# Optimization experiments

Measured on AMD Instinct MI355X. Metric: run time of the kernel, lower is better.

The kernel has to match this reference:

```python
import jax, jax.numpy as jnp
import numpy as np

TAU = 0.07          # temperature
TOP_N_SIM = 5       # n_neighb for KNN label assignment
RANKING_K = 4       # top-k same/diff-class sims for confidence ratio


def setup_inputs() -> dict:
    key = jax.random.key(0)
    k1, k2, k3 = jax.random.split(key, 3)
    n_src, n_tgt, d, n_cls = 8192, 6144, 256, 64
    return {
        "source_features": jax.random.normal(k1, (n_src, d), dtype=jnp.float32),
        "source_labels": jax.random.randint(k2, (n_src,), 0, n_cls, dtype=jnp.int32),
        "target_features": jax.random.normal(k3, (n_tgt, d), dtype=jnp.float32),
    }


def _l2_normalize(x):
    # F.normalize(x, dim=1, p=2) with eps=1e-12
    n = jnp.sqrt(jnp.sum(x * x, axis=1, keepdims=True))
    return x / jnp.maximum(n, 1e-12)


def reference(source_features, source_labels, target_features):
    n_tgt = target_features.shape[0]
    top_ranked_n = n_tgt * 2 // 3

    # cosine similarity matrix [n_src, n_tgt]
    sim = _l2_normalize(source_features) @ _l2_normalize(target_features).T

    # sort each column descending over sources
    order = jnp.argsort(-sim, axis=0)                      # [S, T]

    # KNN label assignment with torch.mode semantics (tie -> smallest value)
    neigh = source_labels[order[:TOP_N_SIM]]               # [K, T]
    counts = (neigh[:, None, :] == neigh[None, :, :]).sum(axis=1)  # [K, T]
    maxc = counts.max(axis=0)                              # [T]
    big = jnp.iinfo(source_labels.dtype).max
    assigned = jnp.where(counts == maxc[None, :], neigh, big).min(axis=0)  # [T]

    # sims & labels reordered by descending similarity, per column
    sorted_sims = jnp.take_along_axis(sim, order, axis=0)  # [S, T]
    sorted_labels = source_labels[order]                   # [S, T]
    pos = sorted_labels == assigned[None, :]               # [S, T]

    def first_k_masked_sum(mask):
        # sum of first RANKING_K sorted sims where mask is True, per column
        csum = jnp.cumsum(mask.astype(sim.dtype), axis=0)
        sel = mask & (csum <= RANKING_K)
        return jnp.sum(jnp.where(sel, sorted_sims, 0.0), axis=0)

    nln = first_k_masked_sum(pos)
    nun = first_k_masked_sum(~pos)
    scores = jax.lax.stop_gradient(nln / nun)              # [T], detached

    _, top_ind = jax.lax.top_k(scores, top_ranked_n)       # confident targets
    conf_sim = sim[:, top_ind]                             # [S, top_ranked_n]
    conf_lab = assigned[top_ind]

    # contrastive softmax loss over sources
    mask_sim = (source_labels[:, None] == conf_lab[None, :]).astype(sim.dtype)
    exp_scores = jax.nn.softmax(conf_sim / TAU, axis=0)
    contrastive = (exp_scores * mask_sim).sum(axis=0) / exp_scores.sum(axis=0)
    return -jnp.mean(jnp.log(contrastive + 1e-6))
```

## Files before the change

### kernel.cpp

```cpp
#include <hip/hip_runtime.h>
#include <cstdint>
#include <cstddef>

#define DIM 256
#define NSRC 8192
#define NCLS 64
#define KSTEPS 8
#define INV_TAU (1.0f / 0.07f)
#define EPITCH 136

typedef __attribute__((ext_vector_type(8))) short bf16x8;
typedef __attribute__((ext_vector_type(4))) float f32x4;
typedef unsigned char uchar;

__device__ __forceinline__ ushort f2bf_rne(float f) {
    uint u = __float_as_uint(f);
    uint r = u + 0x7fff + ((u >> 16) & 1);
    return (ushort)(r >> 16);
}
__device__ __forceinline__ uint bf2ord(uint u) {
    return u ^ (0x8000u + (u >> 15) * 0x7FFFu);
}
__device__ __forceinline__ float ord2f(uint o) {
    uint u = (o & 0x8000u) ? (o ^ 0x8000u) : (~o & 0xFFFFu);
    return __uint_as_float(u << 16);
}

__device__ __forceinline__ void gload_lds16(const void* g, void* l) {
    __builtin_amdgcn_global_load_lds((const __attribute__((address_space(1))) void*)g,
                                     (__attribute__((address_space(3))) void*)l,
                                     16, 0, 0);
}

__global__ __launch_bounds__(256) void l2bf2_k(const float* __restrict__ inA,
                                               ushort* __restrict__ outA, int nA,
                                               const float* __restrict__ inB,
                                               ushort* __restrict__ outB, int nB) {
    const int w = (blockIdx.x * 256 + threadIdx.x) >> 6;
    const int lane = threadIdx.x & 63;
    if (w >= nA + nB) return;
    const float* in;
    ushort* out;
    int row;
    if (w < nA) { in = inA; out = outA; row = w; }
    else        { in = inB; out = outB; row = w - nA; }
    float4 v = *(const float4*)(in + (size_t)row * DIM + lane * 4);
    float ss = v.x * v.x + v.y * v.y + v.z * v.z + v.w * v.w;
#pragma unroll
    for (int d = 1; d < 64; d <<= 1) ss += __shfl_xor(ss, d);
    const float n = fmaxf(sqrtf(ss), 1e-12f);
    ushort4 o;
    o.x = f2bf_rne(v.x / n);
    o.y = f2bf_rne(v.y / n);
    o.z = f2bf_rne(v.z / n);
    o.w = f2bf_rne(v.w / n);
    *(ushort4*)(out + (size_t)row * DIM + lane * 4) = o;
}

__global__ __launch_bounds__(256) void class_build_k(const int* __restrict__ labels,
                                                     uchar* __restrict__ lab8,
                                                     int* __restrict__ cstart,
                                                     int* __restrict__ clist, int n) {
    const int c = blockIdx.x, t = threadIdx.x;
    const int g = c * 256 + t;
    if (g < n) lab8[g] = (uchar)labels[g];

    __shared__ int sl[256], se[256];
    const int per = n >> 8;
    const int i0 = t * per;
    int less = 0, eq = 0;
    for (int j = 0; j < per; ++j) {
        const int l = labels[i0 + j];
        less += (l < c);
        eq += (l == c);
    }
    sl[t] = less; se[t] = eq;
    __syncthreads();
    for (int s = 1; s < 256; s <<= 1) {
        const int a = (t >= s) ? sl[t - s] : 0;
        const int b = (t >= s) ? se[t - s] : 0;
        __syncthreads();
        sl[t] += a; se[t] += b;
        __syncthreads();
    }
    const int base = sl[255];
    int pos = base + se[t] - eq;
    for (int j = 0; j < per; ++j) {
        const int i = i0 + j;
        if (labels[i] == c) clist[pos++] = i;
    }
    if (t == 0) cstart[c] = base;
    if (c == 0 && t == 1) cstart[NCLS] = n;
}

__global__ __launch_bounds__(256) void gemm_mfma_k(const ushort* __restrict__ A,
                                                   const ushort* __restrict__ B,
                                                   ushort* __restrict__ C,
                                                   int M, int N) {
    __shared__ __align__(16) ushort smem[32768];

    const int tid = threadIdx.x;
    const int lane = tid & 63, wid = tid >> 6;
    const int wr = wid >> 1, wc = wid & 1;

    const int nwg = gridDim.x * gridDim.y;
    const int bid = blockIdx.y * gridDim.x + blockIdx.x;
    const int cpx = nwg >> 3;
    const int swzb = (bid & 7) * cpx + (bid >> 3);
    const int bm = (swzb / gridDim.x) * 128;
    const int bn = (swzb % gridDim.x) * 128;

    const char* aSrc[2];
    const char* bSrc[2];
    uint ldsOff[2];
#pragma unroll
    for (int it = 0; it < 2; ++it) {
        const int c = it * 256 + tid;
        const int r = c >> 2;
        const int ch = c & 3;
        const int sch = ch ^ ((r >> 1) & 3);
        aSrc[it] = (const char*)A + (size_t)(bm + r) * (DIM * 2) + sch * 16;
        bSrc[it] = (const char*)B + (size_t)(bn + r) * (DIM * 2) + sch * 16;
        ldsOff[it] = it * 4096 + (uint)(wid * 1024);
    }

    const int fr = lane & 15, fk = lane >> 4;
    const int swz = (fr >> 1) & 3;
    int idxA[4], idxB[4];
#pragma unroll
    for (int m = 0; m < 4; ++m)
        idxA[m] = (wr * 64 + m * 16 + fr) * 32 + ((fk ^ swz) * 8);
#pragma unroll
    for (int n = 0; n < 4; ++n)
        idxB[n] = (wc * 64 + n * 16 + fr) * 32 + ((fk ^ swz) * 8);

    f32x4 acc[4][4];
#pragma unroll
    for (int m = 0; m < 4; ++m)
#pragma unroll
        for (int n = 0; n < 4; ++n) acc[m][n] = (f32x4){0.f, 0.f, 0.f, 0.f};

#define STAGE(b, ks)                                                               \
    {                                                                              \
        _Pragma("unroll") for (int it = 0; it < 2; ++it) {                         \
            gload_lds16(aSrc[it] + (ks) * 64,                                      \
                        (char*)smem + (b) * 8192 + ldsOff[it]);                    \
            gload_lds16(bSrc[it] + (ks) * 64,                                      \
                        (char*)smem + 32768 + (b) * 8192 + ldsOff[it]);            \
        }                                                                          \
    }

    STAGE(0, 0);
    STAGE(1, 1);
    STAGE(2, 2);

#pragma unroll
    for (int ks = 0; ks < KSTEPS; ++ks) {
        if (ks < KSTEPS - 2)      { asm volatile("s_waitcnt vmcnt(8)" ::: "memory"); }
        else if (ks == KSTEPS - 2){ asm volatile("s_waitcnt vmcnt(4)" ::: "memory"); }
        else                      { asm volatile("s_waitcnt vmcnt(0)" ::: "memory"); }
        __builtin_amdgcn_s_barrier();
        asm volatile("" ::: "memory");

        if (ks + 3 < KSTEPS) STAGE((ks + 3) & 3, ks + 3);

        const ushort* sAc = smem + (ks & 3) * 4096;
        const ushort* sBc = smem + 16384 + (ks & 3) * 4096;
        bf16x8 av[4], bv[4];
#pragma unroll
        for (int m = 0; m < 4; ++m) av[m] = *(const bf16x8*)&sAc[idxA[m]];
#pragma unroll
        for (int n = 0; n < 4; ++n) bv[n] = *(const bf16x8*)&sBc[idxB[n]];
#pragma unroll
        for (int m = 0; m < 4; ++m)
#pragma unroll
            for (int n = 0; n < 4; ++n)
                acc[m][n] = __builtin_amdgcn_mfma_f32_16x16x32_bf16(av[m], bv[n], acc[m][n], 0, 0, 0);
    }
#undef STAGE

    __syncthreads();
#pragma unroll
    for (int m = 0; m < 4; ++m) {
#pragma unroll
        for (int n = 0; n < 4; ++n) {
            const int colb = wc * 64 + n * 16 + fr;
#pragma unroll
            for (int j = 0; j < 4; ++j) {
                const int rowb = wr * 64 + m * 16 + fk * 4 + j;
                smem[rowb * EPITCH + colb] = (ushort)bf2ord((uint)f2bf_rne(acc[m][n][j]));
            }
        }
    }
    __syncthreads();
    const int rr = tid >> 4, cc = (tid & 15) * 8;
#pragma unroll
    for (int it = 0; it < 8; ++it) {
        const int r = it * 16 + rr;
        uint4 v = *(const uint4*)&smem[r * EPITCH + cc];
        *(uint4*)(C + (size_t)(bm + r) * N + bn + cc) = v;
    }
}

__global__ __launch_bounds__(256) void assign_score_w(const ushort* __restrict__ sim,
                                                      const int* __restrict__ labels,
                                                      const uchar* __restrict__ lab8,
                                                      const int* __restrict__ cstart,
                                                      const int* __restrict__ clist,
                                                      float* __restrict__ scores_out,
                                                      float* __restrict__ logt_out) {
    const int lane = threadIdx.x & 63, wid = threadIdx.x >> 6;
    const int t = blockIdx.x * 4 + wid;
    const ushort* row = sim + (size_t)t * NSRC;

    uint k0 = 0, k1 = 0, k2 = 0, k3 = 0, k4 = 0, k5 = 0, k6 = 0, k7 = 0;
    float s1 = 0.f;

#define CH4(u16, idx)                                                   \
    {                                                                   \
        uint uu = (uint)(u16);                                          \
        s1 += __expf(fmaf(ord2f(uu), INV_TAU, -INV_TAU));               \
        uint nk = (uu << 16) | (uint)(8191 - (idx));                    \
        uint q;                                                         \
        q = max(k0, nk); nk = min(k0, nk); k0 = q;                      \
        q = max(k1, nk); nk = min(k1, nk); k1 = q;                      \
        q = max(k2, nk); nk = min(k2, nk); k2 = q;                      \
        k3 = max(k3, nk);                                               \
    }
#define CH8(u16, idx)                                                   \
    {                                                                   \
        uint nk = (((uint)(u16)) << 16) | (uint)(8191 - (idx));         \
        uint q;                                                         \
        q = max(k0, nk); nk = min(k0, nk); k0 = q;                      \
        q = max(k1, nk); nk = min(k1, nk); k1 = q;                      \
        q = max(k2, nk); nk = min(k2, nk); k2 = q;                      \
        q = max(k3, nk); nk = min(k3, nk); k3 = q;                      \
        q = max(k4, nk); nk = min(k4, nk); k4 = q;                      \
        q = max(k5, nk); nk = min(k5, nk); k5 = q;                      \
        q = max(k6, nk); nk = min(k6, nk); k6 = q;                      \
        k7 = max(k7, nk);                                               \
    }
#define MERGE8                                                                     \
    _Pragma("unroll")                                                              \
    for (int d = 1; d < 64; d <<= 1) {                                             \
        uint b0 = __shfl_xor(k0, d), b1 = __shfl_xor(k1, d), b2 = __shfl_xor(k2, d),\
             b3 = __shfl_xor(k3, d), b4 = __shfl_xor(k4, d), b5 = __shfl_xor(k5, d),\
             b6 = __shfl_xor(k6, d), b7 = __shfl_xor(k7, d);                        \
        uint r0 = max(k0, b0);                                                     \
        uint r1 = max(max(min(k0, b0), k1), b1);                                   \
        uint r2 = max(max(min(k0, b1), min(k1, b0)), max(k2, b2));                 \
        uint r3 = max(max(min(k0, b2), min(k1, b1)),                               \
                      max(max(min(k2, b0), k3), b3));                              \
        uint r4 = max(max(max(min(k0, b3), min(k1, b2)),                           \
                          max(min(k2, b1), min(k3, b0))), max(k4, b4));            \
        uint r5 = max(max(max(min(k0, b4), min(k1, b3)),                           \
                          max(min(k2, b2), min(k3, b1))),                          \
                      max(max(min(k4, b0), k5), b5));                              \
        uint r6 = max(max(max(min(k0, b5), min(k1, b4)),                           \
                          max(min(k2, b3), min(k3, b2))),                          \
                      max(max(min(k4, b1), min(k5, b0)), max(k6, b6)));            \
        uint r7 = max(max(max(min(k0, b6), min(k1, b5)),                           \
                          max(min(k2, b4), min(k3, b3))),                          \
                      max(max(min(k4, b2), min(k5, b1)),                           \
                          max(max(min(k6, b0), k7), b7)));                         \
        k0 = r0; k1 = r1; k2 = r2; k3 = r3; k4 = r4; k5 = r5; k6 = r6; k7 = r7;    \
    }

    for (int i0 = lane * 8; i0 < NSRC; i0 += 512) {
        uint4 w = *(const uint4*)(row + i0);
        CH4(w.x & 0xFFFF, i0 + 0); CH4(w.x >> 16, i0 + 1);
        CH4(w.y & 0xFFFF, i0 + 2); CH4(w.y >> 16, i0 + 3);
        CH4(w.z & 0xFFFF, i0 + 4); CH4(w.z >> 16, i0 + 5);
        CH4(w.w & 0xFFFF, i0 + 6); CH4(w.w >> 16, i0 + 7);
    }
    const uint prek3 = k3;
    MERGE8;
    if (!__all((int)(prek3 <= k7))) {
        k0 = k1 = k2 = k3 = k4 = k5 = k6 = k7 = 0;
        for (int i0 = lane * 8; i0 < NSRC; i0 += 512) {
            uint4 w = *(const uint4*)(row + i0);
            CH8(w.x & 0xFFFF, i0 + 0); CH8(w.x >> 16, i0 + 1);
            CH8(w.y & 0xFFFF, i0 + 2); CH8(w.y >> 16, i0 + 3);
            CH8(w.z & 0xFFFF, i0 + 4); CH8(w.z >> 16, i0 + 5);
            CH8(w.w & 0xFFFF, i0 + 6); CH8(w.w >> 16, i0 + 7);
        }
        MERGE8;
    }
#undef CH4
#undef CH8
#undef MERGE8

#pragma unroll
    for (int d = 1; d < 64; d <<= 1) s1 += __shfl_xor(s1, d);

    const int l0 = labels[8191 - (int)(k0 & 0xFFFF)];
    const int l1 = labels[8191 - (int)(k1 & 0xFFFF)];
    const int l2 = labels[8191 - (int)(k2 & 0xFFFF)];
    const int l3 = labels[8191 - (int)(k3 & 0xFFFF)];
    const int l4 = labels[8191 - (int)(k4 & 0xFFFF)];
    const int l5 = labels[8191 - (int)(k5 & 0xFFFF)];
    const int l6 = labels[8191 - (int)(k6 & 0xFFFF)];
    const int l7 = labels[8191 - (int)(k7 & 0xFFFF)];

    const int c0 = 1 + (l0 == l1) + (l0 == l2) + (l0 == l3) + (l0 == l4);
    const int c1 = (l1 == l0) + 1 + (l1 == l2) + (l1 == l3) + (l1 == l4);
    const int c2 = (l2 == l0) + (l2 == l1) + 1 + (l2 == l3) + (l2 == l4);
    const int c3 = (l3 == l0) + (l3 == l1) + (l3 == l2) + 1 + (l3 == l4);
    const int c4 = (l4 == l0) + (l4 == l1) + (l4 == l2) + (l4 == l3) + 1;
    const int maxc = max(max(max(c0, c1), max(c2, c3)), c4);
    int assigned = 0x7fffffff;
    if (c0 == maxc) assigned = min(assigned, l0);
    if (c1 == maxc) assigned = min(assigned, l1);
    if (c2 == maxc) assigned = min(assigned, l2);
    if (c3 == maxc) assigned = min(assigned, l3);
    if (c4 == maxc) assigned = min(assigned, l4);
    const int aL = assigned;

    const int negcnt = (l0 != aL) + (l1 != aL) + (l2 != aL) + (l3 != aL) +
                       (l4 != aL) + (l5 != aL) + (l6 != aL) + (l7 != aL);
    float nun = 0.f;
    if (negcnt >= 4) {
        int c = 0;
#define NSTEP(kj, lj)                                                       \
        {                                                                   \
            bool take = ((lj) != aL) && (c < 4);                            \
            nun += take ? ord2f((kj) >> 16) : 0.f;                          \
            c += take ? 1 : 0;                                              \
        }
        NSTEP(k0, l0) NSTEP(k1, l1) NSTEP(k2, l2) NSTEP(k3, l3)
        NSTEP(k4, l4) NSTEP(k5, l5) NSTEP(k6, l6) NSTEP(k7, l7)
#undef NSTEP
    } else {
        uint n0 = 0, n1 = 0, n2 = 0, n3 = 0;
        for (int i0 = lane * 8; i0 < NSRC; i0 += 512) {
            uint4 w = *(const uint4*)(row + i0);
            uint2 lw = *(const uint2*)(lab8 + i0);
#define NEGP(u16, lb)                                                       \
            {                                                               \
                uint x = ((lb) == aL) ? 0u : (uint)(u16);                   \
                uint q;                                                     \
                q = max(n0, x); x = min(n0, x); n0 = q;                     \
                q = max(n1, x); x = min(n1, x); n1 = q;                     \
                q = max(n2, x); x = min(n2, x); n2 = q;                     \
                n3 = max(n3, x);                                            \
            }
            NEGP(w.x & 0xFFFF, (int)(lw.x & 255));
            NEGP(w.x >> 16,    (int)((lw.x >> 8) & 255));
            NEGP(w.y & 0xFFFF, (int)((lw.x >> 16) & 255));
            NEGP(w.y >> 16,    (int)(lw.x >> 24));
            NEGP(w.z & 0xFFFF, (int)(lw.y & 255));
            NEGP(w.z >> 16,    (int)((lw.y >> 8) & 255));
            NEGP(w.w & 0xFFFF, (int)((lw.y >> 16) & 255));
            NEGP(w.w >> 16,    (int)(lw.y >> 24));
#undef NEGP
        }
#pragma unroll
        for (int d = 1; d < 64; d <<= 1) {
            uint b0 = __shfl_xor(n0, d), b1 = __shfl_xor(n1, d),
                 b2 = __shfl_xor(n2, d), b3 = __shfl_xor(n3, d);
            uint r0 = max(n0, b0);
            uint r1 = max(max(min(n0, b0), n1), b1);
            uint r2 = max(max(min(n0, b1), min(n1, b0)), max(n2, b2));
            uint r3 = max(max(min(n0, b2), min(n1, b1)),
                          max(max(min(n2, b0), n3), b3));
            n0 = r0; n1 = r1; n2 = r2; n3 = r3;
        }
        nun = (n0 ? ord2f(n0) : 0.f) + (n1 ? ord2f(n1) : 0.f) +
              (n2 ? ord2f(n2) : 0.f) + (n3 ? ord2f(n3) : 0.f);
    }

    const int cs = cstart[aL], ce = cstart[aL + 1];
    float tp0 = -2.f, tp1 = -2.f, tp2 = -2.f, tp3 = -2.f;
    float sp = 0.f;
    for (int p = cs + lane; p < ce; p += 64) {
        const int idx = clist[p];
        float v = ord2f((uint)row[idx]);
        sp += __expf(fmaf(v, INV_TAU, -INV_TAU));
        float x = v, q;
        q = fmaxf(tp0, x); x = fminf(tp0, x); tp0 = q;
        q = fmaxf(tp1, x); x = fminf(tp1, x); tp1 = q;
        q = fmaxf(tp2, x); x = fminf(tp2, x); tp2 = q;
        tp3 = fmaxf(tp3, x);
    }
#pragma unroll
    for (int d = 1; d < 64; d <<= 1) {
        sp += __shfl_xor(sp, d);
        float b0 = __shfl_xor(tp0, d), b1 = __shfl_xor(tp1, d),
              b2 = __shfl_xor(tp2, d), b3 = __shfl_xor(tp3, d);
        float r0 = fmaxf(tp0, b0);
        float r1 = fmaxf(fmaxf(fminf(tp0, b0), tp1), b1);
        float r2 = fmaxf(fmaxf(fminf(tp0, b1), fminf(tp1, b0)), fmaxf(tp2, b2));
        float r3 = fmaxf(fmaxf(fminf(tp0, b2), fminf(tp1, b1)),
                         fmaxf(fmaxf(fminf(tp2, b0), tp3), b3));
        tp0 = r0; tp1 = r1; tp2 = r2; tp3 = r3;
    }

    if (lane == 0) {
        float nln = (tp0 > -1.5f ? tp0 : 0.f) + (tp1 > -1.5f ? tp1 : 0.f) +
                    (tp2 > -1.5f ? tp2 : 0.f) + (tp3 > -1.5f ? tp3 : 0.f);
        scores_out[t] = nln / nun;
        logt_out[t] = logf(sp / s1 + 1e-6f);
    }
}

__global__ __launch_bounds__(256) void select_topk_w(const float* __restrict__ scores,
                                                     int* __restrict__ selected,
                                                     int n, int k) {
    const int lane = threadIdx.x & 63, wid = threadIdx.x >> 6;
    const int t = blockIdx.x * 4 + wid;
    if (t >= n) return;
    const float st = scores[t];
    int rank = 0;
    for (int j0 = lane * 4; j0 < n; j0 += 256) {
        float4 v = *(const float4*)(scores + j0);
        rank += (v.x > st) || (v.x == st && (j0 + 0) < t);
        rank += (v.y > st) || (v.y == st && (j0 + 1) < t);
        rank += (v.z > st) || (v.z == st && (j0 + 2) < t);
        rank += (v.w > st) || (v.w == st && (j0 + 3) < t);
    }
    for (int d = 1; d < 64; d <<= 1) rank += __shfl_xor(rank, d);
    if (lane == 0) selected[t] = (rank < k) ? 1 : 0;
}

__global__ __launch_bounds__(256) void finalize_k(const float* __restrict__ logt,
                                                  const int* __restrict__ selected,
                                                  float* __restrict__ out, int n, int k) {
    __shared__ float red[256];
    const int tid = threadIdx.x;
    float s = 0.f;
    for (int i = tid; i < n; i += 256) s += selected[i] ? logt[i] : 0.f;
    red[tid] = s;
    __syncthreads();
    for (int st = 128; st > 0; st >>= 1) {
        if (tid < st) red[tid] += red[tid + st];
        __syncthreads();
    }
    if (tid == 0) out[0] = -red[0] / (float)k;
}

extern "C" void kernel_launch(void* const* d_in, const int* in_sizes, int n_in,
                              void* d_out, int out_size, void* d_ws, size_t ws_size,
                              hipStream_t stream) {
    const float* srcF = (const float*)d_in[0];
    const int* labels = (const int*)d_in[1];
    const float* tgtF = (const float*)d_in[2];
    float* out = (float*)d_out;

    const int n_src = in_sizes[1];
    const int d = in_sizes[0] / n_src;
    const int n_tgt = in_sizes[2] / d;
    const int topn = n_tgt * 2 / 3;

    char* ws = (char*)d_ws;
    ushort* src2 = (ushort*)ws;  ws += (size_t)n_src * DIM * sizeof(ushort);
    ushort* tgt2 = (ushort*)ws;  ws += (size_t)n_tgt * DIM * sizeof(ushort);
    ushort* sim  = (ushort*)ws;  ws += (size_t)n_tgt * NSRC * sizeof(ushort);
    float* scores = (float*)ws;  ws += (size_t)n_tgt * sizeof(float);
    float* logt   = (float*)ws;  ws += (size_t)n_tgt * sizeof(float);
    int* selected = (int*)ws;    ws += (size_t)n_tgt * sizeof(int);
    int* cstart   = (int*)ws;    ws += (size_t)(NCLS + 1) * sizeof(int);
    int* clist    = (int*)ws;    ws += (size_t)n_src * sizeof(int);
    uchar* lab8   = (uchar*)ws;  ws += (size_t)n_src;

    const int nrows = n_tgt + n_src;
    l2bf2_k<<<(nrows + 3) / 4, 256, 0, stream>>>(tgtF, tgt2, n_tgt, srcF, src2, n_src);
    class_build_k<<<NCLS, 256, 0, stream>>>(labels, lab8, cstart, clist, n_src);

    dim3 grid(n_src / 128, n_tgt / 128);
    gemm_mfma_k<<<grid, 256, 0, stream>>>(tgt2, src2, sim, n_tgt, n_src);

    assign_score_w<<<n_tgt / 4, 256, 0, stream>>>(sim, labels, lab8, cstart, clist,
                                                  scores, logt);
    select_topk_w<<<(n_tgt + 3) / 4, 256, 0, stream>>>(scores, selected, n_tgt, topn);
    finalize_k<<<1, 256, 0, stream>>>(logt, selected, out, n_tgt, topn);
}
```

Baseline: 128.9 us.

## Load A operands directly to registers and preload full B tile into LDS

The GEMM now streams the A operand straight from global memory into registers with a four-stage rolling prefetch, and copies the whole K extent of the B tile into LDS up front behind a single barrier, replacing the per-step staged A/B LDS pipeline. The block-to-tile mapping is changed to grouped per-XCD tiles to improve L2 reuse, and launch bounds request two blocks per CU. This removes per-k-step barriers and LDS traffic for A, at the cost of more VGPRs, unswizzled global loads for A, and losing overlap of B loading with compute.

New measurement: 142.3 us. 10.4% more time.

```diff
diff --git a/kernel.cpp b/kernel.cpp
--- a/kernel.cpp
+++ b/kernel.cpp
@@ -93,24 +93,28 @@
     if (c == 0 && t == 1) cstart[NCLS] = n;
 }
 
-__global__ __launch_bounds__(256) void gemm_mfma_k(const ushort* __restrict__ A,
-                                                   const ushort* __restrict__ B,
-                                                   ushort* __restrict__ C,
-                                                   int M, int N) {
+__global__ __launch_bounds__(256, 2) void gemm_mfma_k(const ushort* __restrict__ A,
+                                                      const ushort* __restrict__ B,
+                                                      ushort* __restrict__ C,
+                                                      int M, int N) {
     __shared__ __align__(16) ushort smem[32768];
 
     const int tid = threadIdx.x;
     const int lane = tid & 63, wid = tid >> 6;
     const int wr = wid >> 1, wc = wid & 1;
 
-    const int nwg = gridDim.x * gridDim.y;
-    const int bid = blockIdx.y * gridDim.x + blockIdx.x;
-    const int cpx = nwg >> 3;
-    const int swzb = (bid & 7) * cpx + (bid >> 3);
-    const int bm = (swzb / gridDim.x) * 128;
-    const int bn = (swzb % gridDim.x) * 128;
-
-    const char* aSrc[2];
+    const int gx = gridDim.x;
+    const int bid = blockIdx.y * gx + blockIdx.x;
+    const int rowsPerX = gridDim.y >> 3;
+    const int grpW = 8;
+    const int grpSize = rowsPerX * grpW;
+    const int xcd = bid & 7;
+    const int local = bid >> 3;
+    const int grp = local / grpSize;
+    const int within = local % grpSize;
+    const int bm = (xcd * rowsPerX + within % rowsPerX) * 128;
+    const int bn = (grp * grpW + within / rowsPerX) * 128;
+
     const char* bSrc[2];
     uint ldsOff[2];
 #pragma unroll
@@ -119,17 +123,31 @@
         const int r = c >> 2;
         const int ch = c & 3;
         const int sch = ch ^ ((r >> 1) & 3);
-        aSrc[it] = (const char*)A + (size_t)(bm + r) * (DIM * 2) + sch * 16;
         bSrc[it] = (const char*)B + (size_t)(bn + r) * (DIM * 2) + sch * 16;
         ldsOff[it] = it * 4096 + (uint)(wid * 1024);
     }
 
+#pragma unroll
+    for (int ks = 0; ks < KSTEPS; ++ks)
+#pragma unroll
+        for (int it = 0; it < 2; ++it)
+            gload_lds16(bSrc[it] + ks * 64, (char*)smem + ks * 8192 + ldsOff[it]);
+
     const int fr = lane & 15, fk = lane >> 4;
+    const ushort* aPtr[4];
+#pragma unroll
+    for (int m = 0; m < 4; ++m)
+        aPtr[m] = A + (size_t)(bm + wr * 64 + m * 16 + fr) * DIM + fk * 8;
+
+    bf16x8 av[4][4];
+#pragma unroll
+    for (int p = 0; p < 4; ++p)
+#pragma unroll
+        for (int m = 0; m < 4; ++m)
+            av[p][m] = *(const bf16x8*)(aPtr[m] + p * 32);
+
     const int swz = (fr >> 1) & 3;
-    int idxA[4], idxB[4];
-#pragma unroll
-    for (int m = 0; m < 4; ++m)
-        idxA[m] = (wr * 64 + m * 16 + fr) * 32 + ((fk ^ swz) * 8);
+    int idxB[4];
 #pragma unroll
     for (int n = 0; n < 4; ++n)
         idxB[n] = (wc * 64 + n * 16 + fr) * 32 + ((fk ^ swz) * 8);
@@ -140,44 +158,25 @@
 #pragma unroll
         for (int n = 0; n < 4; ++n) acc[m][n] = (f32x4){0.f, 0.f, 0.f, 0.f};
 
-#define STAGE(b, ks)                                                               \
-    {                                                                              \
-        _Pragma("unroll") for (int it = 0; it < 2; ++it) {                         \
-            gload_lds16(aSrc[it] + (ks) * 64,                                      \
-                        (char*)smem + (b) * 8192 + ldsOff[it]);                    \
-            gload_lds16(bSrc[it] + (ks) * 64,                                      \
-                        (char*)smem + 32768 + (b) * 8192 + ldsOff[it]);            \
-        }                                                                          \
-    }
-
-    STAGE(0, 0);
-    STAGE(1, 1);
-    STAGE(2, 2);
+    __syncthreads();
 
 #pragma unroll
     for (int ks = 0; ks < KSTEPS; ++ks) {
-        if (ks < KSTEPS - 2)      { asm volatile("s_waitcnt vmcnt(8)" ::: "memory"); }
-        else if (ks == KSTEPS - 2){ asm volatile("s_waitcnt vmcnt(4)" ::: "memory"); }
-        else                      { asm volatile("s_waitcnt vmcnt(0)" ::: "memory"); }
-        __builtin_amdgcn_s_barrier();
-        asm volatile("" ::: "memory");
-
-        if (ks + 3 < KSTEPS) STAGE((ks + 3) & 3, ks + 3);
-
-        const ushort* sAc = smem + (ks & 3) * 4096;
-        const ushort* sBc = smem + 16384 + (ks & 3) * 4096;
-        bf16x8 av[4], bv[4];
-#pragma unroll
-        for (int m = 0; m < 4; ++m) av[m] = *(const bf16x8*)&sAc[idxA[m]];
+        const ushort* sBc = smem + ks * 4096;
+        bf16x8 bv[4];
 #pragma unroll
         for (int n = 0; n < 4; ++n) bv[n] = *(const bf16x8*)&sBc[idxB[n]];
 #pragma unroll
         for (int m = 0; m < 4; ++m)
 #pragma unroll
             for (int n = 0; n < 4; ++n)
-                acc[m][n] = __builtin_amdgcn_mfma_f32_16x16x32_bf16(av[m], bv[n], acc[m][n], 0, 0, 0);
-    }
-#undef STAGE
+                acc[m][n] = __builtin_amdgcn_mfma_f32_16x16x32_bf16(av[ks & 3][m], bv[n], acc[m][n], 0, 0, 0);
+        if (ks + 4 < KSTEPS) {
+#pragma unroll
+            for (int m = 0; m < 4; ++m)
+                av[ks & 3][m] = *(const bf16x8*)(aPtr[m] + (ks + 4) * 32);
+        }
+    }
 
     __syncthreads();
 #pragma unroll
```
